# Performance work log

Measured on AMD Instinct MI355X. Metric: run time of the kernel, lower is better.

## Reference

```python
import jax, jax.numpy as jnp
import numpy as np

EPS = 1e-6
SCAL = 5.0
PARTS = 16
NFEAT = 32
RES = 64


def conv(x, w, b, stride=1):
    y = jax.lax.conv_general_dilated(x, w, (stride, stride), 'SAME',
                                     dimension_numbers=('NCHW', 'OIHW', 'NCHW'))
    return y + b[None, :, None, None]


def spatial_softmax(x):
    b, k, h, w = x.shape
    return jax.nn.softmax(x.reshape(b, k, h * w), axis=-1).reshape(b, k, h, w)


def make_grid(h, w):
    ys = jnp.linspace(-1.0, 1.0, h)
    xs = jnp.linspace(-1.0, 1.0, w)
    gy, gx = jnp.meshgrid(ys, xs, indexing='ij')
    return jnp.stack([gy, gx], axis=-1)  # [h, w, 2]


def e_sigma(x, w1, b1, w2, b2, wp, bp):
    # shared shape/appearance encoder: parts via spatial softmax + residual sum map
    h1 = jax.nn.relu(conv(x, w1, b1, stride=2))   # [B,64,64,64]
    h2 = jax.nn.relu(conv(h1, w2, b2))            # [B,64,64,64]
    parts = spatial_softmax(conv(h2, wp, bp))     # [B,16,64,64]
    return parts, h2


def e_alpha(x, w1, b1, w2, b2):
    h1 = jax.nn.relu(conv(x, w1, b1))
    return conv(h1, w2, b2)                       # [B,32,64,64]


def get_mu_and_prec(parts):
    # soft-argmax mean + 2x2 covariance -> inverse Cholesky factor L_inv
    b, k, h, w = parts.shape
    grid = make_grid(h, w)
    mu = jnp.einsum('bkhw,hwc->bkc', parts, grid)                       # [b,k,2]
    outer = jnp.einsum('hwm,hwn->hwmn', grid, grid)
    cov = jnp.einsum('bkhw,hwmn->bkmn', parts, outer) - jnp.einsum('bkm,bkn->bkmn', mu, mu)
    a = jnp.sqrt(cov[..., 0, 0] + EPS)
    bb = cov[..., 0, 1] / (a + EPS)
    c = jnp.sqrt(jnp.maximum(cov[..., 1, 1] - bb * bb, 0.0) + EPS)
    det = a * c
    z = jnp.zeros_like(a)
    L_inv = SCAL / (det[..., None, None] + EPS) * jnp.stack(
        [jnp.stack([c, z], axis=-1), jnp.stack([-bb, a], axis=-1)], axis=-2)  # [b,k,2,2]
    return mu, L_inv


def feat_mu_to_enc(alpha, mu, L_inv, h, w):
    # render Cauchy-shaped part heatmaps from (mu, L_inv) and paint part features
    grid = make_grid(h, w)
    dist = grid[None, None] - mu[:, :, None, None, :]        # [b,k,h,w,2]
    proj = jnp.einsum('bkhwi,bkij->bkhwj', dist, L_inv)
    heat = 1.0 / (1.0 + jnp.sum(proj * proj, axis=-1))       # [b,k,h,w]
    norm = heat / (jnp.sum(heat, axis=(2, 3), keepdims=True) + EPS)
    fmap = jnp.einsum('bkf,bkhw->bfhw', alpha, norm)         # [b,nf,h,w]
    return jnp.concatenate([heat, fmap], axis=1)             # [b,nk+nf,h,w]


def decoder(enc, w1, b1, w2, b2, w3, b3):
    h1 = jax.nn.relu(conv(enc, w1, b1))                      # [B,64,64,64]
    up = jnp.repeat(jnp.repeat(h1, 2, axis=2), 2, axis=3)    # nearest upsample -> 128
    h2 = jax.nn.relu(conv(up, w2, b2))
    return jax.nn.sigmoid(conv(h2, w3, b3))                  # [B,3,128,128]


def setup_inputs():
    key = jax.random.key(0)
    ks = jax.random.split(key, 16)
    def w(k, shape):
        fan_in = shape[1] * shape[2] * shape[3]
        return (jax.random.normal(k, shape, jnp.float32) / np.sqrt(fan_in)).astype(jnp.float32)
    B = 32
    return {
        'x': jax.random.uniform(ks[0], (B, 3, 128, 128), jnp.float32),
        'x_spatial_transform': jax.random.uniform(ks[1], (B, 3, 128, 128), jnp.float32),
        'x_appearance_transform': jax.random.uniform(ks[2], (B, 3, 128, 128), jnp.float32),
        'coord': jax.random.normal(ks[3], (B, PARTS, 2), jnp.float32) * 0.5,
        'vector': jax.random.normal(ks[4], (B, PARTS, 2), jnp.float32) * 0.1,
        'es_w1': w(ks[5], (RES, 3, 3, 3)), 'es_b1': jnp.zeros((RES,), jnp.float32),
        'es_w2': w(ks[6], (RES, RES, 3, 3)), 'es_b2': jnp.zeros((RES,), jnp.float32),
        'es_wp': w(ks[7], (PARTS, RES, 3, 3)), 'es_bp': jnp.zeros((PARTS,), jnp.float32),
        'ea_w1': w(ks[8], (RES, RES, 3, 3)), 'ea_b1': jnp.zeros((RES,), jnp.float32),
        'ea_w2': w(ks[9], (NFEAT, RES, 3, 3)), 'ea_b2': jnp.zeros((NFEAT,), jnp.float32),
        'd_w1': w(ks[10], (RES, PARTS + NFEAT, 3, 3)), 'd_b1': jnp.zeros((RES,), jnp.float32),
        'd_w2': w(ks[11], (32, RES, 3, 3)), 'd_b2': jnp.zeros((32,), jnp.float32),
        'd_w3': w(ks[12], (3, 32, 3, 3)), 'd_b3': jnp.zeros((3,), jnp.float32),
    }


def reference(x, x_spatial_transform, x_appearance_transform, coord, vector,
              es_w1, es_b1, es_w2, es_b2, es_wp, es_bp,
              ea_w1, ea_b1, ea_w2, ea_b2,
              d_w1, d_b1, d_w2, d_b2, d_w3, d_b3):
    # shape stream (appearance-transformed image -> geometry)
    shape_parts, _ = e_sigma(x_appearance_transform, es_w1, es_b1, es_w2, es_b2, es_wp, es_bp)
    mu, L_inv = get_mu_and_prec(shape_parts)
    # appearance stream (spatially-transformed image -> appearance)
    app_parts, app_sum = e_sigma(x_spatial_transform, es_w1, es_b1, es_w2, es_b2, es_wp, es_bp)
    f_xs = e_alpha(app_sum, ea_w1, ea_b1, ea_w2, ea_b2)
    # local part appearances: gather features under each part map
    alpha = jnp.einsum('bfhw,bkhw->bkf', f_xs, app_parts)
    encoding = feat_mu_to_enc(alpha, mu, L_inv, 64, 64)
    reconstruction = decoder(encoding, d_w1, d_b1, d_w2, d_b2, d_w3, d_b3)
    # composite loss
    mu_a, L_inv_a = get_mu_and_prec(app_parts)
    rec_loss = jnp.mean((x - reconstruction) ** 2)
    equiv_loss = jnp.mean((mu - mu_a) ** 2) + 0.01 * jnp.mean((L_inv - L_inv_a) ** 2)
    transport_loss = jnp.mean((mu_a - (coord + vector)) ** 2)
    loss = rec_loss + equiv_loss + transport_loss
    return reconstruction, loss
```

## Files before the change

### kernel.cpp

```cpp
#include <hip/hip_runtime.h>
#include <hip/hip_bf16.h>

#define EPS 1e-6f
#define SCAL 5.0f

typedef __attribute__((ext_vector_type(8))) short bf8v;
typedef __attribute__((ext_vector_type(4))) float f32x4;

#define OFF_MU     0
#define OFF_LINV   1024
#define OFF_MUA    3072
#define OFF_LINVA  4096
#define OFF_HSUM   6144
#define OFF_ALPHA  6656
#define OFF_REC    23040
#define OFF_R1     32768
#define OFF_R2     (OFF_R1 + 8388608)
#define OFF_R3     (OFF_R2 + 8388608)
#define WS_TOTAL   (OFF_R3 + 16777216)

#define BA_XA   ((size_t)2 * OFF_R3)
#define BA_X2   ((size_t)2 * OFF_R1)
#define OFF_PARTSF OFF_R2
#define OFF_PROBS  (OFF_R2 + 4194304)
#define BA_EA1  ((size_t)2 * OFF_R3)
#define OFF_FXS (OFF_R3 + 4194304)
#define BA_E    ((size_t)2 * OFF_R2)
#define BA_D1   ((size_t)2 * OFF_R1)
#define BA_D2   ((size_t)2 * OFF_R3)

#define WT_ESW1 0
#define WT_ESB1 1728
#define WT_ESB2 1792
#define WT_ESBP 1856
#define WT_EAB1 1872
#define WT_EAB2 1936
#define WT_DB1  1968
#define WT_DB2  2032
#define WT_W3P  2064
#define WT_DB3  2928
#define P_WP2  0
#define P_WPP  36864
#define P_WPA1 46080
#define P_WPA2 82944
#define P_WPD1 101376
#define P_WPD2 138240

__device__ __attribute__((aligned(16))) float g_ws[WS_TOTAL];
__device__ __attribute__((aligned(16))) float g_wt[3072];
__device__ __attribute__((aligned(16))) __hip_bfloat16 g_wp[156672];
__device__ int g_isbf16;

__device__ __forceinline__ float selz(bool c, float v) { return c ? v : 0.f; }
__device__ __forceinline__ float cvtbf(short s) {
    return __uint_as_float(((unsigned int)(unsigned short)s) << 16);
}
__device__ __forceinline__ short f2bf(float f) {
    unsigned u = __float_as_uint(f);
    u += 0x7fff + ((u >> 16) & 1);
    return (short)(u >> 16);
}
__device__ __forceinline__ float ldin(const void* p, size_t i, int bf) {
    return bf ? __bfloat162float(((const __hip_bfloat16*)p)[i])
              : ((const float*)p)[i];
}

__device__ __forceinline__ float block_sum(float v) {
    __shared__ float sb[8];
    for (int off = 32; off; off >>= 1) v += __shfl_down(v, off, 64);
    int lane = threadIdx.x & 63, wid = threadIdx.x >> 6;
    __syncthreads();
    if (lane == 0) sb[wid] = v;
    __syncthreads();
    float r = 0.f;
    for (int i = 0; i < 4; ++i) r += sb[i];
    return r;
}
__device__ __forceinline__ float block_max(float v) {
    __shared__ float sb[8];
    for (int off = 32; off; off >>= 1) v = fmaxf(v, __shfl_down(v, off, 64));
    int lane = threadIdx.x & 63, wid = threadIdx.x >> 6;
    __syncthreads();
    if (lane == 0) sb[wid] = v;
    __syncthreads();
    float r = -1e30f;
    for (int i = 0; i < 4; ++i) r = fmaxf(r, sb[i]);
    return r;
}

__global__ void detect_k(const void* x) {
    const __hip_bfloat16* p = (const __hip_bfloat16*)x;
    int lane = threadIdx.x & 63;
    float v = 0.f;
    for (int i = lane; i < 256; i += 64) {
        float a = fabsf(__bfloat162float(p[i]));
        if (!(a <= 2.0f)) v = 1.f;
    }
    for (int off = 32; off; off >>= 1) v += __shfl_down(v, off, 64);
    if (lane == 0) {
        g_isbf16 = (v == 0.f) ? 1 : 0;
        g_ws[OFF_REC] = 0.f;
    }
}

__global__ void wpack_k(const void* esw1, const void* esb1, const void* esw2, const void* esb2,
                        const void* eswp, const void* esbp, const void* eaw1, const void* eab1,
                        const void* eaw2, const void* eab2, const void* dw1, const void* db1,
                        const void* dw2, const void* db2, const void* dw3, const void* db3) {
    int bf = g_isbf16;
    int gid0 = blockIdx.x * 256 + threadIdx.x, stride = gridDim.x * 256;
    for (int g = gid0; g < 512; g += stride) g_ws[OFF_HSUM + g] = 0.f;
    for (int g = gid0; g < 1728; g += stride) g_wt[WT_ESW1 + g] = ldin(esw1, g, bf);
    for (int g = gid0; g < 64; g += stride) g_wt[WT_ESB1 + g] = ldin(esb1, g, bf);
    for (int g = gid0; g < 64; g += stride) g_wt[WT_ESB2 + g] = ldin(esb2, g, bf);
    for (int g = gid0; g < 16; g += stride) g_wt[WT_ESBP + g] = ldin(esbp, g, bf);
    for (int g = gid0; g < 64; g += stride) g_wt[WT_EAB1 + g] = ldin(eab1, g, bf);
    for (int g = gid0; g < 32; g += stride) g_wt[WT_EAB2 + g] = ldin(eab2, g, bf);
    for (int g = gid0; g < 64; g += stride) g_wt[WT_DB1 + g] = ldin(db1, g, bf);
    for (int g = gid0; g < 32; g += stride) g_wt[WT_DB2 + g] = ldin(db2, g, bf);
    for (int g = gid0; g < 3; g += stride) g_wt[WT_DB3 + g] = ldin(db3, g, bf);
    for (int g = gid0; g < 864; g += stride) {
        int t = g / 96, o = (g / 32) % 3, k = g & 31;
        g_wt[WT_W3P + g] = ldin(dw3, (size_t)(o * 32 + k) * 9 + t, bf);
    }
    for (int g = gid0; g < 36864; g += stride) {
        int t = g >> 12, n = (g >> 6) & 63, k = g & 63;
        g_wp[P_WP2 + g] = __float2bfloat16(ldin(esw2, (size_t)(n * 64 + k) * 9 + t, bf));
    }
    for (int g = gid0; g < 9216; g += stride) {
        int t = g >> 10, n = (g >> 6) & 15, k = g & 63;
        g_wp[P_WPP + g] = __float2bfloat16(ldin(eswp, (size_t)(n * 64 + k) * 9 + t, bf));
    }
    for (int g = gid0; g < 36864; g += stride) {
        int t = g >> 12, n = (g >> 6) & 63, k = g & 63;
        g_wp[P_WPA1 + g] = __float2bfloat16(ldin(eaw1, (size_t)(n * 64 + k) * 9 + t, bf));
    }
    for (int g = gid0; g < 18432; g += stride) {
        int t = g >> 11, n = (g >> 6) & 31, k = g & 63;
        g_wp[P_WPA2 + g] = __float2bfloat16(ldin(eaw2, (size_t)(n * 64 + k) * 9 + t, bf));
    }
    for (int g = gid0; g < 36864; g += stride) {
        int t = g >> 12, n = (g >> 6) & 63, k = g & 63;
        float v = (k < 48) ? ldin(dw1, (size_t)(n * 48 + k) * 9 + t, bf) : 0.f;
        g_wp[P_WPD1 + g] = __float2bfloat16(v);
    }
    for (int g = gid0; g < 18432; g += stride) {
        int t = g >> 11, n = (g >> 6) & 31, k = g & 63;
        g_wp[P_WPD2 + g] = __float2bfloat16(ldin(dw2, (size_t)(n * 64 + k) * 9 + t, bf));
    }
}

__global__ void __launch_bounds__(256)
conv_s2n_k(const void* __restrict__ inA, const void* __restrict__ inB) {
    int bf = g_isbf16;
    int tile = blockIdx.x & 15;
    int gb = blockIdx.x >> 4;
    int g = gb & 3, b = gb >> 2;
    const void* in = (b < 32) ? inA : inB;
    int bb = b & 31;
    int pix = tile * 256 + threadIdx.x;
    int y = pix >> 6, x = pix & 63;
    size_t inb = (size_t)bb * 3 * 16384;
    const float* W = g_wt + WT_ESW1 + (size_t)(g * 16) * 27;
    float acc[16];
    #pragma unroll
    for (int o = 0; o < 16; ++o) acc[o] = g_wt[WT_ESB1 + g * 16 + o];
    int iy0 = 2 * y, ix0 = 2 * x;
    bool my2 = (iy0 + 2 < 128), mx2 = (ix0 + 2 < 128);
    int iy2 = my2 ? iy0 + 2 : 127, ix2 = mx2 ? ix0 + 2 : 127;
    for (int ic = 0; ic < 3; ++ic) {
        size_t pb = inb + ic * 16384;
        float t[9];
        t[0] = ldin(in, pb + iy0 * 128 + ix0, bf);
        t[1] = ldin(in, pb + iy0 * 128 + ix0 + 1, bf);
        t[2] = selz(mx2, ldin(in, pb + iy0 * 128 + ix2, bf));
        t[3] = ldin(in, pb + (iy0 + 1) * 128 + ix0, bf);
        t[4] = ldin(in, pb + (iy0 + 1) * 128 + ix0 + 1, bf);
        t[5] = selz(mx2, ldin(in, pb + (iy0 + 1) * 128 + ix2, bf));
        t[6] = selz(my2, ldin(in, pb + iy2 * 128 + ix0, bf));
        t[7] = selz(my2, ldin(in, pb + iy2 * 128 + ix0 + 1, bf));
        t[8] = selz(my2 && mx2, ldin(in, pb + iy2 * 128 + ix2, bf));
        #pragma unroll
        for (int o = 0; o < 16; ++o) {
            const float* wr = W + (o * 3 + ic) * 9;
            float a = acc[o];
            #pragma unroll
            for (int j = 0; j < 9; ++j) a = fmaf(t[j], wr[j], a);
            acc[o] = a;
        }
    }
    __hip_bfloat16* out = (__hip_bfloat16*)g_ws + BA_XA + ((size_t)b * 4096 + pix) * 64 + g * 16;
    #pragma unroll
    for (int o = 0; o < 16; ++o) out[o] = __float2bfloat16(fmaxf(acc[o], 0.f));
}

template<int TR>
__device__ __forceinline__ void stage_tile(__hip_bfloat16* sA,
                                           const __hip_bfloat16* __restrict__ inb, int y0) {
    for (int g = threadIdx.x; g < TR * 512; g += 256) {
        int r = g >> 9;
        int rem = g & 511;
        int px = rem >> 3, j = rem & 7;
        int yy = y0 - 1 + r;
        int P = px + 1;
        bf8v v = (bf8v){0, 0, 0, 0, 0, 0, 0, 0};
        if (yy >= 0 && yy <= 63)
            v = *(const bf8v*)(inb + ((size_t)(yy * 64 + px) * 64 + j * 8));
        *(bf8v*)(sA + ((r * 66 + P) * 64 + ((j ^ (P & 7)) * 8))) = v;
    }
    if (threadIdx.x < TR * 16) {
        int g = threadIdx.x;
        int r = g >> 4, rem = g & 15, side = rem >> 3, j = rem & 7;
        int P = side ? 65 : 0;
        *(bf8v*)(sA + ((r * 66 + P) * 64 + ((j ^ (P & 7)) * 8))) = (bf8v){0, 0, 0, 0, 0, 0, 0, 0};
    }
}

template<int MS>
__device__ __forceinline__ void ld_a(const __hip_bfloat16* sA, int it, int rowIn,
                                     int l15, int quad, bf8v (&a)[MS]) {
    const int t = it >> 1, c = it & 1;
    const int dy = t / 3 - 1, dx = t % 3 - 1;
    const int r = rowIn + 1 + dy;
    const int j = c * 4 + quad;
    #pragma unroll
    for (int ms = 0; ms < MS; ++ms) {
        int P = ms * 16 + l15 + dx + 1;
        a[ms] = *(const bf8v*)(sA + ((r * 66 + P) * 64 + ((j ^ (P & 7)) * 8)));
    }
}
template<int MS>
__device__ __forceinline__ void ld_a2(const __hip_bfloat16* sA, int it, int rowbase,
                                      int l15, int quad, bf8v (&a)[2][MS]) {
    const int t = it >> 1, c = it & 1;
    const int dy = t / 3 - 1, dx = t % 3 - 1;
    const int j = c * 4 + quad;
    #pragma unroll
    for (int rp = 0; rp < 2; ++rp) {
        const int r = rowbase + rp + 1 + dy;
        #pragma unroll
        for (int ms = 0; ms < MS; ++ms) {
            int P = ms * 16 + l15 + dx + 1;
            a[rp][ms] = *(const bf8v*)(sA + ((r * 66 + P) * 64 + ((j ^ (P & 7)) * 8)));
        }
    }
}
template<int TOTN, int NS>
__device__ __forceinline__ void ld_b(int it, int ocoff, int l15, int quad, int wp_off,
                                     bf8v (&bv)[NS]) {
    const int t = it >> 1, c = it & 1;
    #pragma unroll
    for (int ns = 0; ns < NS; ++ns)
        bv[ns] = *(const bf8v*)(g_wp + wp_off +
                 ((size_t)(t * TOTN + ocoff + ns * 16 + l15) * 64 + c * 32 + quad * 8));
}

template<int TOTN, int NS, int MS>
__device__ __forceinline__ void conv_body(const __hip_bfloat16* sA, int rowIn,
                                          int l15, int quad, int wp_off,
                                          f32x4 (&acc)[MS][NS]) {
    bf8v bq[3][NS];
    bf8v a[2][MS];
    ld_b<TOTN, NS>(0, 0, l15, quad, wp_off, bq[0]);
    ld_b<TOTN, NS>(1, 0, l15, quad, wp_off, bq[1]);
    ld_a<MS>(sA, 0, rowIn, l15, quad, a[0]);
    #pragma unroll
    for (int it = 0; it < 18; ++it) {
        if (it + 2 < 18) ld_b<TOTN, NS>(it + 2, 0, l15, quad, wp_off, bq[(it + 2) % 3]);
        if (it + 1 < 18) ld_a<MS>(sA, it + 1, rowIn, l15, quad, a[(it + 1) & 1]);
        #pragma unroll
        for (int ns = 0; ns < NS; ++ns)
            #pragma unroll
            for (int ms = 0; ms < MS; ++ms)
                acc[ms][ns] = __builtin_amdgcn_mfma_f32_16x16x32_bf16(
                    a[it & 1][ms], bq[it % 3][ns], acc[ms][ns], 0, 0, 0);
    }
}

template<int TOTN, int NSW, int MS>
__device__ __forceinline__ void conv_body2(const __hip_bfloat16* sA, int rowbase, int ocoff,
                                           int l15, int quad, int wp_off,
                                           f32x4 (&acc)[2][MS][NSW]) {
    bf8v bq[3][NSW];
    bf8v a[2][2][MS];
    ld_b<TOTN, NSW>(0, ocoff, l15, quad, wp_off, bq[0]);
    ld_b<TOTN, NSW>(1, ocoff, l15, quad, wp_off, bq[1]);
    ld_a2<MS>(sA, 0, rowbase, l15, quad, a[0]);
    #pragma unroll
    for (int it = 0; it < 18; ++it) {
        if (it + 2 < 18) ld_b<TOTN, NSW>(it + 2, ocoff, l15, quad, wp_off, bq[(it + 2) % 3]);
        if (it + 1 < 18) ld_a2<MS>(sA, it + 1, rowbase, l15, quad, a[(it + 1) & 1]);
        #pragma unroll
        for (int rp = 0; rp < 2; ++rp)
            #pragma unroll
            for (int ns = 0; ns < NSW; ++ns)
                #pragma unroll
                for (int ms = 0; ms < MS; ++ms)
                    acc[rp][ms][ns] = __builtin_amdgcn_mfma_f32_16x16x32_bf16(
                        a[it & 1][rp][ms], bq[it % 3][ns], acc[rp][ms][ns], 0, 0, 0);
    }
}

template<int TOTN, int NSW, int OUTF32, int RELU>
__device__ __forceinline__ void epi_2r(f32x4 (&acc)[2][4][NSW], int bO, int y0, int rowbase,
                                       int ocoff, int l15, int quad, int bias_off,
                                       size_t out_off) {
    #pragma unroll
    for (int rp = 0; rp < 2; ++rp) {
        int y = y0 + rowbase + rp;
        #pragma unroll
        for (int ns = 0; ns < NSW; ++ns) {
            float bias = g_wt[bias_off + ocoff + ns * 16 + l15];
            #pragma unroll
            for (int ms = 0; ms < 4; ++ms) {
                #pragma unroll
                for (int r = 0; r < 4; ++r) {
                    int pix = ms * 16 + quad * 4 + r;
                    float v = acc[rp][ms][ns][r] + bias;
                    if (RELU) v = fmaxf(v, 0.f);
                    size_t o = out_off + ((size_t)(bO * 4096 + y * 64 + pix)) * TOTN +
                               ocoff + ns * 16 + l15;
                    if (OUTF32) g_ws[o] = v;
                    else ((__hip_bfloat16*)g_ws)[o] = __float2bfloat16(v);
                }
            }
        }
    }
}

template<int TOTN, int NSW, int OUTF32, int RELU>
__global__ void __launch_bounds__(256) __attribute__((amdgpu_waves_per_eu(2, 3)))
conv_mfl_k(size_t in_off, int wp_off, int bias_off, size_t out_off) {
    __shared__ __hip_bfloat16 sA[6 * 66 * 64];
    int wid = threadIdx.x >> 6, lane = threadIdx.x & 63;
    int l15 = lane & 15, quad = lane >> 4;
    int b = blockIdx.x >> 4, y0 = (blockIdx.x & 15) * 4;
    int og = wid & 1, rowbase = (wid >> 1) * 2;
    int ocoff = og * NSW * 16;
    const __hip_bfloat16* inb = (const __hip_bfloat16*)g_ws + in_off + (size_t)b * 4096 * 64;
    stage_tile<6>(sA, inb, y0);
    __syncthreads();
    f32x4 acc[2][4][NSW];
    #pragma unroll
    for (int rp = 0; rp < 2; ++rp)
        #pragma unroll
        for (int ms = 0; ms < 4; ++ms)
            #pragma unroll
            for (int ns = 0; ns < NSW; ++ns) acc[rp][ms][ns] = (f32x4){0.f, 0.f, 0.f, 0.f};
    conv_body2<TOTN, NSW, 4>(sA, rowbase, ocoff, l15, quad, wp_off, acc);
    epi_2r<TOTN, NSW, OUTF32, RELU>(acc, b, y0, rowbase, ocoff, l15, quad, bias_off, out_off);
}

__global__ void __launch_bounds__(256) __attribute__((amdgpu_waves_per_eu(2, 3)))
conv_pea_k() {
    __shared__ __hip_bfloat16 sA[6 * 66 * 64];
    int wid = threadIdx.x >> 6, lane = threadIdx.x & 63;
    int l15 = lane & 15, quad = lane >> 4;
    int b = blockIdx.x & 63;
    int y0 = (int)(blockIdx.x >> 6) * 4;
    const __hip_bfloat16* inb = (const __hip_bfloat16*)g_ws + BA_X2 + (size_t)b * 4096 * 64;
    stage_tile<6>(sA, inb, y0);
    __syncthreads();
    f32x4 accP[4][1];
    #pragma unroll
    for (int ms = 0; ms < 4; ++ms) accP[ms][0] = (f32x4){0.f, 0.f, 0.f, 0.f};
    conv_body<16, 1, 4>(sA, wid, l15, quad, P_WPP, accP);
    if (b >= 32) {
        int og = wid & 1, rowbase = (wid >> 1) * 2;
        int ocoff = og * 32;
        f32x4 accE[2][4][2];
        #pragma unroll
        for (int rp = 0; rp < 2; ++rp)
            #pragma unroll
            for (int ms = 0; ms < 4; ++ms)
                #pragma unroll
                for (int ns = 0; ns < 2; ++ns) accE[rp][ms][ns] = (f32x4){0.f, 0.f, 0.f, 0.f};
        conv_body2<64, 2, 4>(sA, rowbase, ocoff, l15, quad, P_WPA1, accE);
        epi_2r<64, 2, 0, 1>(accE, b - 32, y0, rowbase, ocoff, l15, quad, WT_EAB1, BA_EA1);
    }
    __syncthreads();
    float* tb = (float*)sA;
    float biasP = g_wt[WT_ESBP + l15];
    #pragma unroll
    for (int ms = 0; ms < 4; ++ms)
        #pragma unroll
        for (int r = 0; r < 4; ++r)
            tb[l15 * 260 + wid * 64 + ms * 16 + quad * 4 + r] = accP[ms][0][r] + biasP;
    __syncthreads();
    int k = threadIdx.x >> 4, xo = (threadIdx.x & 15) * 16;
    float* dst = g_ws + OFF_PARTSF + ((size_t)(b * 16 + k)) * 4096 + y0 * 64 + xo;
    const float* src = tb + k * 260 + xo;
    #pragma unroll
    for (int i = 0; i < 16; i += 4)
        *(f32x4*)(dst + i) = *(const f32x4*)(src + i);
}

__global__ void __launch_bounds__(256) __attribute__((amdgpu_waves_per_eu(2, 3)))
conv_upmf2_k(size_t in_off, int wp_off, int bias_off, size_t out_off) {
    __shared__ __hip_bfloat16 sA[4 * 66 * 64];
    int wid = threadIdx.x >> 6, lane = threadIdx.x & 63;
    int l15 = lane & 15, quad = lane >> 4;
    int b = blockIdx.x >> 5, y0 = (blockIdx.x & 31) * 4;
    int ri0 = (y0 >> 1) - 1;
    const __hip_bfloat16* inb = (const __hip_bfloat16*)g_ws + in_off + (size_t)b * 4096 * 64;
    for (int g = threadIdx.x; g < 2048; g += 256) {
        int r = g >> 9;
        int rem = g & 511;
        int px = rem >> 3, j = rem & 7;
        int yi = ri0 + r;
        int P = px + 1;
        bf8v v = (bf8v){0, 0, 0, 0, 0, 0, 0, 0};
        if (yi >= 0 && yi <= 63)
            v = *(const bf8v*)(inb + ((size_t)(yi * 64 + px) * 64 + j * 8));
        *(bf8v*)(sA + ((r * 66 + P) * 64 + ((j ^ (P & 7)) * 8))) = v;
    }
    if (threadIdx.x < 64) {
        int g = threadIdx.x;
        int r = g >> 4, rem = g & 15, side = rem >> 3, j = rem & 7;
        int P = side ? 65 : 0;
        *(bf8v*)(sA + ((r * 66 + P) * 64 + ((j ^ (P & 7)) * 8))) = (bf8v){0, 0, 0, 0, 0, 0, 0, 0};
    }
    __syncthreads();
    int og = wid & 1, rowbase = (wid >> 1) * 2;
    f32x4 acc[2][8];
    #pragma unroll
    for (int rp = 0; rp < 2; ++rp)
        #pragma unroll
        for (int ms = 0; ms < 8; ++ms) acc[rp][ms] = (f32x4){0.f, 0.f, 0.f, 0.f};
    bf8v bq[3][1];
    ld_b<32, 1>(0, og * 16, l15, quad, wp_off, bq[0]);
    ld_b<32, 1>(1, og * 16, l15, quad, wp_off, bq[1]);
    #pragma unroll
    for (int it = 0; it < 18; ++it) {
        if (it + 2 < 18) ld_b<32, 1>(it + 2, og * 16, l15, quad, wp_off, bq[(it + 2) % 3]);
        const int t = it >> 1, c = it & 1;
        const int dy = t / 3 - 1, dx = t % 3 - 1;
        #pragma unroll
        for (int rp = 0; rp < 2; ++rp) {
            int yy = y0 + rowbase + rp + dy;
            if (yy >= 0 && yy <= 127) {
                int r = (yy >> 1) - ri0;
                int j = c * 4 + quad;
                bf8v a[8];
                #pragma unroll
                for (int ms = 0; ms < 8; ++ms) {
                    int xx = ms * 16 + l15 + dx;
                    int P = (xx < 0) ? 0 : ((xx > 127) ? 65 : ((xx >> 1) + 1));
                    a[ms] = *(const bf8v*)(sA + ((r * 66 + P) * 64 + ((j ^ (P & 7)) * 8)));
                }
                #pragma unroll
                for (int ms = 0; ms < 8; ++ms)
                    acc[rp][ms] = __builtin_amdgcn_mfma_f32_16x16x32_bf16(a[ms], bq[it % 3][0], acc[rp][ms], 0, 0, 0);
            }
        }
    }
    float bias = g_wt[bias_off + og * 16 + l15];
    #pragma unroll
    for (int rp = 0; rp < 2; ++rp) {
        int y = y0 + rowbase + rp;
        #pragma unroll
        for (int ms = 0; ms < 8; ++ms) {
            #pragma unroll
            for (int r = 0; r < 4; ++r) {
                int pix = ms * 16 + quad * 4 + r;
                float v = fmaxf(acc[rp][ms][r] + bias, 0.f);
                size_t o = out_off + ((size_t)(b * 16384 + y * 128 + pix)) * 32 + og * 16 + l15;
                ((__hip_bfloat16*)g_ws)[o] = __float2bfloat16(v);
            }
        }
    }
}

__global__ void sm_mom3_k() {
    int bk = blockIdx.x;
    int b = bk >> 4;
    int app = (b >= 32);
    const float* P = g_ws + OFF_PARTSF + (size_t)bk * 4096;
    float r[16];
    #pragma unroll
    for (int j = 0; j < 16; ++j) r[j] = P[threadIdx.x + j * 256];
    float m = r[0];
    #pragma unroll
    for (int j = 1; j < 16; ++j) m = fmaxf(m, r[j]);
    m = block_max(m);
    float s = 0.f;
    #pragma unroll
    for (int j = 0; j < 16; ++j) { r[j] = __expf(r[j] - m); s += r[j]; }
    s = block_sum(s);
    float inv = 1.0f / s;
    float sy = 0, sx = 0, syy = 0, sxy = 0, sxx = 0;
    #pragma unroll
    for (int j = 0; j < 16; ++j) {
        float pv = r[j] * inv;
        int i = threadIdx.x + j * 256;
        if (app) g_ws[OFF_PROBS + (size_t)(bk - 512) * 4096 + i] = pv;
        float gy = -1.0f + (i >> 6) * (2.0f / 63.0f);
        float gx = -1.0f + (i & 63) * (2.0f / 63.0f);
        sy += pv * gy; sx += pv * gx;
        syy += pv * gy * gy; sxy += pv * gy * gx; sxx += pv * gx * gx;
    }
    sy = block_sum(sy); sx = block_sum(sx);
    syy = block_sum(syy); sxy = block_sum(sxy); sxx = block_sum(sxx);
    if (threadIdx.x == 0) {
        float c00 = syy - sy * sy, c01 = sxy - sy * sx, c11 = sxx - sx * sx;
        float a = sqrtf(fmaxf(c00 + EPS, 1e-12f));
        float bb = c01 / (a + EPS);
        float cc = sqrtf(fmaxf(c11 - bb * bb, 0.f) + EPS);
        float det = a * cc;
        float sc = SCAL / (det + EPS);
        int idx = app ? (bk - 512) : bk;
        int mu_off = app ? OFF_MUA : OFF_MU;
        int linv_off = app ? OFF_LINVA : OFF_LINV;
        g_ws[mu_off + idx * 2 + 0] = sy;
        g_ws[mu_off + idx * 2 + 1] = sx;
        g_ws[linv_off + idx * 4 + 0] = cc * sc;
        g_ws[linv_off + idx * 4 + 1] = 0.f;
        g_ws[linv_off + idx * 4 + 2] = -bb * sc;
        g_ws[linv_off + idx * 4 + 3] = a * sc;
    }
}

__global__ void alpha2_k() {
    int b = blockIdx.x & 31, k = blockIdx.x >> 5;
    int bk = b * 16 + k;
    __shared__ float pl[4096];
    const float* pr = g_ws + OFF_PROBS + (size_t)bk * 4096;
    for (int i = threadIdx.x; i < 4096; i += 256) pl[i] = pr[i];
    __syncthreads();
    float acc[32];
    #pragma unroll
    for (int f = 0; f < 32; ++f) acc[f] = 0.f;
    for (int i = threadIdx.x; i < 4096; i += 256) {
        float pv = pl[i];
        const float* fp = g_ws + OFF_FXS + (size_t)(b * 4096 + i) * 32;
        #pragma unroll
        for (int f = 0; f < 32; ++f) acc[f] = fmaf(pv, fp[f], acc[f]);
    }
    __shared__ float sw[4][32];
    int lane = threadIdx.x & 63, wid = threadIdx.x >> 6;
    #pragma unroll
    for (int f = 0; f < 32; ++f)
        for (int off = 32; off; off >>= 1) acc[f] += __shfl_down(acc[f], off, 64);
    if (lane == 0) {
        #pragma unroll
        for (int f = 0; f < 32; ++f) sw[wid][f] = acc[f];
    }
    __syncthreads();
    if (threadIdx.x < 32)
        g_ws[OFF_ALPHA + bk * 32 + threadIdx.x] =
            sw[0][threadIdx.x] + sw[1][threadIdx.x] + sw[2][threadIdx.x] + sw[3][threadIdx.x];
}

__global__ void heat2_k() {
    int tile = blockIdx.x & 15, b = blockIdx.x >> 4;
    __shared__ float hs[16];
    if (threadIdx.x < 16) hs[threadIdx.x] = 0.f;
    __syncthreads();
    int pix = tile * 256 + threadIdx.x;
    float gy = -1.0f + (pix >> 6) * (2.0f / 63.0f);
    float gx = -1.0f + (pix & 63) * (2.0f / 63.0f);
    bf8v e0, e1;
    float hv[16];
    #pragma unroll
    for (int k = 0; k < 16; ++k) {
        int bk = b * 16 + k;
        float m0 = g_ws[OFF_MU + bk * 2], m1 = g_ws[OFF_MU + bk * 2 + 1];
        float L00 = g_ws[OFF_LINV + bk * 4 + 0], L10 = g_ws[OFF_LINV + bk * 4 + 2],
              L11 = g_ws[OFF_LINV + bk * 4 + 3];
        float d0 = gy - m0, d1 = gx - m1;
        float p0 = d0 * L00 + d1 * L10;
        float p1 = d1 * L11;
        float h = 1.0f / (1.0f + p0 * p0 + p1 * p1);
        hv[k] = h;
        short sbits = f2bf(h);
        if (k < 8) e0[k] = sbits; else e1[k - 8] = sbits;
    }
    __hip_bfloat16* E = (__hip_bfloat16*)g_ws + BA_E + (size_t)(b * 4096 + pix) * 64;
    *(bf8v*)E = e0;
    *(bf8v*)(E + 8) = e1;
    #pragma unroll
    for (int k = 0; k < 16; ++k) {
        float v = hv[k];
        for (int off = 32; off; off >>= 1) v += __shfl_down(v, off, 64);
        if ((threadIdx.x & 63) == 0) atomicAdd(&hs[k], v);
    }
    __syncthreads();
    if (threadIdx.x < 16)
        atomicAdd(&g_ws[OFF_HSUM + b * 16 + threadIdx.x], hs[threadIdx.x]);
}

__global__ void fmap2_k() {
    int tile = blockIdx.x & 15, b = blockIdx.x >> 4;
    __shared__ float coef[16][32];
    for (int i = threadIdx.x; i < 512; i += 256) {
        int k = i >> 5, f = i & 31;
        coef[k][f] = g_ws[OFF_ALPHA + (b * 16 + k) * 32 + f] /
                     (g_ws[OFF_HSUM + b * 16 + k] + EPS);
    }
    __syncthreads();
    int pix = tile * 256 + threadIdx.x;
    __hip_bfloat16* E = (__hip_bfloat16*)g_ws + BA_E + (size_t)(b * 4096 + pix) * 64;
    float h[16];
    #pragma unroll
    for (int k = 0; k < 16; ++k) h[k] = __bfloat162float(E[k]);
    #pragma unroll
    for (int f = 0; f < 32; ++f) {
        float a = 0.f;
        #pragma unroll
        for (int k = 0; k < 16; ++k) a = fmaf(h[k], coef[k][f], a);
        E[16 + f] = __float2bfloat16(a);
    }
    #pragma unroll
    for (int z = 48; z < 64; ++z) E[z] = __float2bfloat16(0.f);
}

__device__ __forceinline__ void ld_tap9(const short* __restrict__ D2, int y, int x, int t,
                                        bf8v (&dst)[4]) {
    int dy = t / 3 - 1, dx = t % 3 - 1;
    int yy = y + dy, xx = x + dx;
    bool ok = ((unsigned)yy < 128u) && ((unsigned)xx < 128u);
    const short* sp = D2 + (size_t)((ok ? yy : y) * 128 + (ok ? xx : x)) * 32;
    const bf8v zv = (bf8v){0, 0, 0, 0, 0, 0, 0, 0};
    #pragma unroll
    for (int c = 0; c < 4; ++c) {
        bf8v tmp = *(const bf8v*)(sp + c * 8);
        dst[c] = ok ? tmp : zv;
    }
}
__device__ __forceinline__ void fma_tap(const bf8v (&v)[4], int t, float (&acc)[3]) {
    #pragma unroll
    for (int c = 0; c < 4; ++c)
        #pragma unroll
        for (int j = 0; j < 8; ++j) {
            float av = cvtbf(v[c][j]);
            int kk = c * 8 + j;
            acc[0] = fmaf(av, g_wt[WT_W3P + (t * 3 + 0) * 32 + kk], acc[0]);
            acc[1] = fmaf(av, g_wt[WT_W3P + (t * 3 + 1) * 32 + kk], acc[1]);
            acc[2] = fmaf(av, g_wt[WT_W3P + (t * 3 + 2) * 32 + kk], acc[2]);
        }
}
__global__ void __launch_bounds__(256)
conv_sign_k(const void* __restrict__ ximg, void* __restrict__ outp) {
    int bf = g_isbf16;
    int tile = blockIdx.x & 63, b = blockIdx.x >> 6;
    int pix = tile * 256 + threadIdx.x;
    int y = pix >> 7, x = pix & 127;
    const short* D2 = (const short*)((const __hip_bfloat16*)g_ws + BA_D2 + (size_t)b * 16384 * 32);
    float acc[3];
    #pragma unroll
    for (int o = 0; o < 3; ++o) acc[o] = g_wt[WT_DB3 + o];
    bf8v vA[4], vB[4];
    ld_tap9(D2, y, x, 0, vA);
    #pragma unroll 1
    for (int tt = 0; tt < 4; ++tt) {
        int t0 = 2 * tt, t1 = 2 * tt + 1;
        ld_tap9(D2, y, x, t1, vB);
        fma_tap(vA, t0, acc);
        ld_tap9(D2, y, x, t1 + 1, vA);
        fma_tap(vB, t1, acc);
    }
    fma_tap(vA, 8, acc);
    float es = 0.f;
    #pragma unroll
    for (int o = 0; o < 3; ++o) {
        float v = 1.0f / (1.0f + __expf(-acc[o]));
        size_t oidx = ((size_t)b * 3 + o) * 16384 + pix;
        if (bf) ((__hip_bfloat16*)outp)[oidx] = __float2bfloat16(v);
        else    ((float*)outp)[oidx] = v;
        float e = ldin(ximg, oidx, bf) - v;
        es += e * e;
    }
    float s = block_sum(es);
    if (threadIdx.x == 0) atomicAdd(&g_ws[OFF_REC], s);
}

__global__ void loss_k(const void* __restrict__ coord,
                       const void* __restrict__ vec,
                       void* __restrict__ outp) {
    int bf = g_isbf16;
    const float* mu = g_ws + OFF_MU;
    const float* linv = g_ws + OFF_LINV;
    const float* mu_a = g_ws + OFF_MUA;
    const float* linv_a = g_ws + OFF_LINVA;
    float s1 = 0, s2 = 0, s3 = 0;
    for (int i = threadIdx.x; i < 1024; i += 256) {
        float d = mu[i] - mu_a[i];
        s1 += d * d;
        float t = ldin(coord, i, bf) + ldin(vec, i, bf);
        float d3 = mu_a[i] - t;
        s3 += d3 * d3;
    }
    for (int i = threadIdx.x; i < 2048; i += 256) {
        float d = linv[i] - linv_a[i];
        s2 += d * d;
    }
    s1 = block_sum(s1);
    s2 = block_sum(s2);
    s3 = block_sum(s3);
    if (threadIdx.x == 0) {
        float loss = g_ws[OFF_REC] / 1572864.0f + s1 / 1024.0f + 0.01f * (s2 / 2048.0f)
                   + s3 / 1024.0f;
        if (bf) ((__hip_bfloat16*)outp)[1572864] = __float2bfloat16(loss);
        else    ((float*)outp)[1572864] = loss;
    }
}

extern "C" void kernel_launch(void* const* d_in, const int* in_sizes, int n_in,
                              void* d_out, int out_size, void* d_ws, size_t ws_size,
                              hipStream_t stream) {
    const void* x     = d_in[0];
    const void* x_st  = d_in[1];
    const void* x_at  = d_in[2];
    const void* coord = d_in[3];
    const void* vec   = d_in[4];

    dim3 blk(256);

    detect_k<<<1, 64, 0, stream>>>(x);
    wpack_k<<<64, blk, 0, stream>>>(
        d_in[5],  d_in[6],  d_in[7],  d_in[8],
        d_in[9],  d_in[10], d_in[11], d_in[12],
        d_in[13], d_in[14], d_in[15], d_in[16],
        d_in[17], d_in[18], d_in[19], d_in[20]);

    conv_s2n_k<<<64 * 4 * 16, blk, 0, stream>>>(x_at, x_st);
    conv_mfl_k<64, 2, 0, 1><<<1024, blk, 0, stream>>>(BA_XA, P_WP2, WT_ESB2, BA_X2);

    conv_pea_k<<<1024, blk, 0, stream>>>();
    sm_mom3_k<<<1024, blk, 0, stream>>>();

    conv_mfl_k<32, 1, 1, 0><<<512, blk, 0, stream>>>(BA_EA1, P_WPA2, WT_EAB2, (size_t)OFF_FXS);
    alpha2_k<<<512, blk, 0, stream>>>();

    heat2_k<<<512, blk, 0, stream>>>();
    fmap2_k<<<512, blk, 0, stream>>>();

    conv_mfl_k<64, 2, 0, 1><<<512, blk, 0, stream>>>(BA_E, P_WPD1, WT_DB1, BA_D1);
    conv_upmf2_k<<<1024, blk, 0, stream>>>(BA_D1, P_WPD2, WT_DB2, BA_D2);
    conv_sign_k<<<32 * 64, blk, 0, stream>>>(x, d_out);

    loss_k<<<1, blk, 0, stream>>>(coord, vec, d_out);
}
```

Baseline: 388.6 us.

## Repack conv weights per K-chunk and compute all 64 channels per thread in stride-2 conv

Packed weight layout changes so each (tap, K-half) chunk stores 32 contiguous input channels per output channel, making MFMA B-operand loads contiguous over a smaller stride. The first stride-2 conv now computes all 64 output channels per thread instead of splitting into four 16-channel groups, so the input taps are loaded once rather than four times, at the cost of 4x fewer blocks and much higher register pressure (64 accumulators).

Measured after the change: 385.7 us. Within noise of the previous version (-0.8%).

```diff
diff --git a/kernel.cpp b/kernel.cpp
--- a/kernel.cpp
+++ b/kernel.cpp
@@ -124,28 +124,34 @@
         g_wt[WT_W3P + g] = ldin(dw3, (size_t)(o * 32 + k) * 9 + t, bf);
     }
     for (int g = gid0; g < 36864; g += stride) {
-        int t = g >> 12, n = (g >> 6) & 63, k = g & 63;
+        int kk = g & 31, n = (g >> 5) & 63, tc = g >> 11;
+        int t = tc >> 1, k = (tc & 1) * 32 + kk;
         g_wp[P_WP2 + g] = __float2bfloat16(ldin(esw2, (size_t)(n * 64 + k) * 9 + t, bf));
     }
     for (int g = gid0; g < 9216; g += stride) {
-        int t = g >> 10, n = (g >> 6) & 15, k = g & 63;
+        int kk = g & 31, n = (g >> 5) & 15, tc = g >> 9;
+        int t = tc >> 1, k = (tc & 1) * 32 + kk;
         g_wp[P_WPP + g] = __float2bfloat16(ldin(eswp, (size_t)(n * 64 + k) * 9 + t, bf));
     }
     for (int g = gid0; g < 36864; g += stride) {
-        int t = g >> 12, n = (g >> 6) & 63, k = g & 63;
+        int kk = g & 31, n = (g >> 5) & 63, tc = g >> 11;
+        int t = tc >> 1, k = (tc & 1) * 32 + kk;
         g_wp[P_WPA1 + g] = __float2bfloat16(ldin(eaw1, (size_t)(n * 64 + k) * 9 + t, bf));
     }
     for (int g = gid0; g < 18432; g += stride) {
-        int t = g >> 11, n = (g >> 6) & 31, k = g & 63;
+        int kk = g & 31, n = (g >> 5) & 31, tc = g >> 10;
+        int t = tc >> 1, k = (tc & 1) * 32 + kk;
         g_wp[P_WPA2 + g] = __float2bfloat16(ldin(eaw2, (size_t)(n * 64 + k) * 9 + t, bf));
     }
     for (int g = gid0; g < 36864; g += stride) {
-        int t = g >> 12, n = (g >> 6) & 63, k = g & 63;
+        int kk = g & 31, n = (g >> 5) & 63, tc = g >> 11;
+        int t = tc >> 1, k = (tc & 1) * 32 + kk;
         float v = (k < 48) ? ldin(dw1, (size_t)(n * 48 + k) * 9 + t, bf) : 0.f;
         g_wp[P_WPD1 + g] = __float2bfloat16(v);
     }
     for (int g = gid0; g < 18432; g += stride) {
-        int t = g >> 11, n = (g >> 6) & 31, k = g & 63;
+        int kk = g & 31, n = (g >> 5) & 31, tc = g >> 10;
+        int t = tc >> 1, k = (tc & 1) * 32 + kk;
         g_wp[P_WPD2 + g] = __float2bfloat16(ldin(dw2, (size_t)(n * 64 + k) * 9 + t, bf));
     }
 }
@@ -154,17 +160,15 @@
 conv_s2n_k(const void* __restrict__ inA, const void* __restrict__ inB) {
     int bf = g_isbf16;
     int tile = blockIdx.x & 15;
-    int gb = blockIdx.x >> 4;
-    int g = gb & 3, b = gb >> 2;
+    int b = blockIdx.x >> 4;
     const void* in = (b < 32) ? inA : inB;
     int bb = b & 31;
     int pix = tile * 256 + threadIdx.x;
     int y = pix >> 6, x = pix & 63;
     size_t inb = (size_t)bb * 3 * 16384;
-    const float* W = g_wt + WT_ESW1 + (size_t)(g * 16) * 27;
-    float acc[16];
-    #pragma unroll
-    for (int o = 0; o < 16; ++o) acc[o] = g_wt[WT_ESB1 + g * 16 + o];
+    float acc[64];
+    #pragma unroll
+    for (int o = 0; o < 64; ++o) acc[o] = g_wt[WT_ESB1 + o];
     int iy0 = 2 * y, ix0 = 2 * x;
     bool my2 = (iy0 + 2 < 128), mx2 = (ix0 + 2 < 128);
     int iy2 = my2 ? iy0 + 2 : 127, ix2 = mx2 ? ix0 + 2 : 127;
@@ -181,17 +185,17 @@
         t[7] = selz(my2, ldin(in, pb + iy2 * 128 + ix0 + 1, bf));
         t[8] = selz(my2 && mx2, ldin(in, pb + iy2 * 128 + ix2, bf));
         #pragma unroll
-        for (int o = 0; o < 16; ++o) {
-            const float* wr = W + (o * 3 + ic) * 9;
+        for (int o = 0; o < 64; ++o) {
+            const float* wr = g_wt + WT_ESW1 + (o * 3 + ic) * 9;
             float a = acc[o];
             #pragma unroll
             for (int j = 0; j < 9; ++j) a = fmaf(t[j], wr[j], a);
             acc[o] = a;
         }
     }
-    __hip_bfloat16* out = (__hip_bfloat16*)g_ws + BA_XA + ((size_t)b * 4096 + pix) * 64 + g * 16;
-    #pragma unroll
-    for (int o = 0; o < 16; ++o) out[o] = __float2bfloat16(fmaxf(acc[o], 0.f));
+    __hip_bfloat16* out = (__hip_bfloat16*)g_ws + BA_XA + ((size_t)b * 4096 + pix) * 64;
+    #pragma unroll
+    for (int o = 0; o < 64; ++o) out[o] = __float2bfloat16(fmaxf(acc[o], 0.f));
 }
 
 template<int TR>
@@ -248,11 +252,10 @@
 template<int TOTN, int NS>
 __device__ __forceinline__ void ld_b(int it, int ocoff, int l15, int quad, int wp_off,
                                      bf8v (&bv)[NS]) {
-    const int t = it >> 1, c = it & 1;
     #pragma unroll
     for (int ns = 0; ns < NS; ++ns)
         bv[ns] = *(const bf8v*)(g_wp + wp_off +
-                 ((size_t)(t * TOTN + ocoff + ns * 16 + l15) * 64 + c * 32 + quad * 8));
+                 ((size_t)(it * TOTN + ocoff + ns * 16 + l15) * 32 + quad * 8));
 }
 
 template<int TOTN, int NS, int MS>
@@ -723,7 +726,7 @@
         d_in[13], d_in[14], d_in[15], d_in[16],
         d_in[17], d_in[18], d_in[19], d_in[20]);
 
-    conv_s2n_k<<<64 * 4 * 16, blk, 0, stream>>>(x_at, x_st);
+    conv_s2n_k<<<64 * 16, blk, 0, stream>>>(x_at, x_st);
     conv_mfl_k<64, 2, 0, 1><<<1024, blk, 0, stream>>>(BA_XA, P_WP2, WT_ESB2, BA_X2);
 
     conv_pea_k<<<1024, blk, 0, stream>>>();
```
